# Kernel tuning notes

Hardware: AMD Instinct MI355X
Metric: run time of the kernel (lower is better)

Reference implementation:

```python
import jax, jax.numpy as jnp
import numpy as np

L, P, B, C, H, W = 2, 2, 4, 128, 64, 64
K = 2  # negatives per sample


def setup_inputs() -> dict:
    key = jax.random.key(0)
    k1, k2, k3, k4, k5 = jax.random.split(key, 5)
    shp = (L, P, B, C, H, W)
    return {
        "style_E": jax.random.normal(k1, shp, dtype=jnp.float32),
        "style_S": jax.random.normal(k2, shp, dtype=jnp.float32),
        "translate_E": jax.random.normal(k3, shp, dtype=jnp.float32),
        "translate_S": jax.random.normal(k4, shp, dtype=jnp.float32),
        "neg_idx": jax.random.randint(k5, (B, K), 0, B, dtype=jnp.int32),
    }


def reference(style_E, style_S, translate_E, translate_S, neg_idx):
    # Stack E and S levels: [2L, P, B, C, N] with N = H*W
    S = jnp.concatenate([style_E, style_S], axis=0).reshape(2 * L, P, B, C, -1)
    T = jnp.concatenate([translate_E, translate_S], axis=0).reshape(2 * L, P, B, C, -1)

    # EFDM: sort style values; permute them to trans's rank order, then MSE.
    Vs = jnp.sort(S, axis=-1)                      # value_style
    idx_t = jnp.argsort(T, axis=-1)                # index_trans
    inv = jnp.argsort(idx_t, axis=-1)              # inverse_index

    # Positive pairs: style[b] vs trans[b]
    matched_pos = jnp.take_along_axis(Vs, inv, axis=-1)
    # mse over (C, N) per slice (matches mse_loss on a [1,C,N] tensor)
    pos = jnp.mean((T - matched_pos) ** 2, axis=(3, 4))  # [2L, P, B]
    poss_loss = pos.sum(axis=(0, 1))                      # [B]

    # Negatives: style[nb] vs trans[b] for nb in neg_idx[b]
    Vs_neg = Vs[:, :, neg_idx]                            # [2L, P, B, K, C, N]
    matched_neg = jnp.take_along_axis(Vs_neg, inv[:, :, :, None], axis=-1)
    neg = jnp.mean((T[:, :, :, None] - matched_neg) ** 2, axis=(4, 5))  # [2L, P, B, K]
    neg_loss = neg.sum(axis=(0, 1, 3))                    # [B]

    return jnp.sum(poss_loss / neg_loss)
```

## Files before the change

kernel.cpp:

```cpp
#include <hip/hip_runtime.h>


typedef unsigned int u32;
typedef __fp16 f16x2 __attribute__((ext_vector_type(2)));

constexpr int N     = 4096;
constexpr int NTH   = 256;
constexpr int CDIM  = 128;
constexpr int BDIM  = 4;
constexpr int KNEG  = 2;
constexpr int ROWS  = 4096;
constexpr int HALF  = 2048;
constexpr int LSTRW = 20;
constexpr int ROWW  = N / 2;

__device__ inline u32 pk_min(u32 a, u32 b) {
  u32 d; asm("v_pk_min_f16 %0, %1, %2" : "=v"(d) : "v"(a), "v"(b)); return d;
}
__device__ inline u32 pk_max(u32 a, u32 b) {
  u32 d; asm("v_pk_max_f16 %0, %1, %2" : "=v"(d) : "v"(a), "v"(b)); return d;
}
__device__ inline u32 pk_min_swap(u32 a) {
  u32 d; asm("v_pk_min_f16 %0, %1, %1 op_sel:[0,1] op_sel_hi:[1,0]" : "=v"(d) : "v"(a)); return d;
}
__device__ inline u32 pk_max_swap(u32 a) {
  u32 d; asm("v_pk_max_f16 %0, %1, %1 op_sel:[0,1] op_sel_hi:[1,0]" : "=v"(d) : "v"(a)); return d;
}
__device__ inline u32 pk_sub(u32 a, u32 b) {
  u32 d; asm("v_pk_add_f16 %0, %1, %2 neg_lo:[0,1] neg_hi:[0,1]" : "=v"(d) : "v"(a), "v"(b)); return d;
}
__device__ inline float dot2acc(u32 d, float acc) {
  asm("v_dot2_f32_f16 %0, %1, %2, %0" : "+v"(acc) : "v"(d), "v"(d)); return acc;
}

__device__ inline void pk_cswap(u32& a, u32& b) {
  const u32 mn = pk_min(a, b), mx = pk_max(a, b);
  a = mn; b = mx;
}
__device__ inline u32 pk_sort_pair(u32 a) {
  const u32 mn = pk_min_swap(a);
  const u32 mx = pk_max_swap(a);
  return (mx & 0xFFFF0000u) | (mn & 0x0000FFFFu);
}

__device__ inline void cswap_asc(float& a, float& b) {
  const float lo = fminf(a, b), hi = fmaxf(a, b);
  a = lo; b = hi;
}
template<int K, int J>
__device__ inline void local_pass(float v[16]) {
  #pragma unroll
  for (int m = 0; m < 16; ++m)
    if ((m & J) == 0) {
      if ((m & K) == 0) cswap_asc(v[m], v[m ^ J]);
      else              cswap_asc(v[m ^ J], v[m]);
    }
}

template<int CTRL>
__device__ inline u32 dpp_u(u32 x) {
  return (u32)__builtin_amdgcn_update_dpp((int)x, (int)x, CTRL, 0xF, 0xF, false);
}

template<int TM>
__device__ inline void pass_small_pk(u32 h[8], int t) {
  const bool km = ((t & TM) == 0);
  u32 o[8];
  #pragma unroll
  for (int p = 0; p < 8; ++p) {
    if constexpr (TM == 1)      o[p] = dpp_u<0xB1>(h[p]);
    else if constexpr (TM == 2) o[p] = dpp_u<0x4E>(h[p]);
    else if constexpr (TM == 4) o[p] = dpp_u<0x141>(dpp_u<0x1B>(h[p]));
    else                        o[p] = dpp_u<0x128>(h[p]);
  }
  #pragma unroll
  for (int p = 0; p < 8; ++p) {
    const u32 mn = pk_min(h[p], o[p]), mx = pk_max(h[p], o[p]);
    h[p] = km ? mn : mx;
  }
}

__device__ inline void swap32u(u32& a, u32& b) {
  asm("v_permlane32_swap_b32 %0, %1" : "+v"(a), "+v"(b));
}
__device__ inline void swap16u(u32& a, u32& b) {
  asm("v_permlane16_swap_b32 %0, %1" : "+v"(a), "+v"(b));
}
template<bool IS32>
__device__ inline void pass_perm_pk(u32 h[8]) {
  #pragma unroll
  for (int q = 0; q < 4; ++q) {
    u32 a = h[2*q], b = h[2*q + 1];
    if constexpr (IS32) swap32u(a, b); else swap16u(a, b);
    u32 mn = pk_min(a, b);
    u32 mx = pk_max(a, b);
    if constexpr (IS32) swap32u(mn, mx); else swap16u(mn, mx);
    h[2*q] = mn; h[2*q + 1] = mx;
  }
}

template<int TM>
__device__ inline void pass_lds_pk(u32 h[8], u32* buf, int t) {
  __syncthreads();
  uint4* wp = (uint4*)(buf + t * LSTRW);
  wp[0] = make_uint4(h[0], h[1], h[2], h[3]);
  wp[1] = make_uint4(h[4], h[5], h[6], h[7]);
  __syncthreads();
  const uint4* rp = (const uint4*)(buf + (t ^ TM) * LSTRW);
  const uint4 x0 = rp[0], x1 = rp[1];
  if (t & TM) {
    h[0] = pk_max(h[0], x0.x); h[1] = pk_max(h[1], x0.y);
    h[2] = pk_max(h[2], x0.z); h[3] = pk_max(h[3], x0.w);
    h[4] = pk_max(h[4], x1.x); h[5] = pk_max(h[5], x1.y);
    h[6] = pk_max(h[6], x1.z); h[7] = pk_max(h[7], x1.w);
  } else {
    h[0] = pk_min(h[0], x0.x); h[1] = pk_min(h[1], x0.y);
    h[2] = pk_min(h[2], x0.z); h[3] = pk_min(h[3], x0.w);
    h[4] = pk_min(h[4], x1.x); h[5] = pk_min(h[5], x1.y);
    h[6] = pk_min(h[6], x1.z); h[7] = pk_min(h[7], x1.w);
  }
}

template<int K, int J>
__device__ inline void cross_pk(u32 h[8], u32* buf, int t) {
  if constexpr (J >= 16) {
    constexpr int TM = J >> 4;
    if constexpr (TM >= 64)      pass_lds_pk<TM>(h, buf, t);
    else if constexpr (TM == 32) pass_perm_pk<true>(h);
    else if constexpr (TM == 16) pass_perm_pk<false>(h);
    else                         pass_small_pk<TM>(h, t);
    cross_pk<K, (J >> 1)>(h, buf, t);
  }
}

__device__ inline void tail_pk(u32 h[8]) {
  #pragma unroll
  for (int p = 0; p < 8; ++p) h[p] = pk_sort_pair(h[p]);
  pk_cswap(h[0], h[4]); pk_cswap(h[1], h[5]); pk_cswap(h[2], h[6]); pk_cswap(h[3], h[7]);
  pk_cswap(h[0], h[2]); pk_cswap(h[1], h[3]); pk_cswap(h[4], h[6]); pk_cswap(h[5], h[7]);
  pk_cswap(h[0], h[1]); pk_cswap(h[2], h[3]); pk_cswap(h[4], h[5]); pk_cswap(h[6], h[7]);
}

__device__ inline void flip_pk(u32 h[8], u32 f) {
  #pragma unroll
  for (int p = 0; p < 8; ++p) h[p] ^= f;
}

template<int K>
__device__ inline void stage_pk(u32 h[8], u32* buf, int t, u32& cur) {
  const u32 f = (t & (K >> 4)) ? 0x80008000u : 0u;
  flip_pk(h, f ^ cur);
  cur = f;
  cross_pk<K, (K >> 1)>(h, buf, t);
  tail_pk(h);
}

__device__ inline void load_prestage_pack(const float* __restrict__ src,
                                          u32 h[8], int t) {
  float v[16];
  const float4* s4 = (const float4*)src;
  #pragma unroll
  for (int q = 0; q < 4; ++q) {
    const float4 x = s4[t * 4 + q];
    v[q*4+0] = x.x; v[q*4+1] = x.y; v[q*4+2] = x.z; v[q*4+3] = x.w;
  }
  local_pass<2, 1>(v);
  local_pass<4, 2>(v); local_pass<4, 1>(v);
  local_pass<8, 4>(v); local_pass<8, 2>(v); local_pass<8, 1>(v);
  #pragma unroll
  for (int p = 0; p < 8; ++p) {
    const f16x2 pk = __builtin_amdgcn_cvt_pkrtz(v[p], v[p + 8]);
    h[p] = __builtin_bit_cast(u32, pk);
  }
}

__device__ inline void sort4096_pk(u32 h[8], u32* buf, int t) {
  u32 cur = 0;
  stage_pk<16>(h, buf, t, cur);
  stage_pk<32>(h, buf, t, cur);
  stage_pk<64>(h, buf, t, cur);
  stage_pk<128>(h, buf, t, cur);
  stage_pk<256>(h, buf, t, cur);
  stage_pk<512>(h, buf, t, cur);
  stage_pk<1024>(h, buf, t, cur);
  stage_pk<2048>(h, buf, t, cur);
  stage_pk<4096>(h, buf, t, cur);
}

__device__ inline void store_row(u32* __restrict__ dst, const u32 h[8], int t) {
  uint4* d4 = (uint4*)dst;
  d4[t*2]     = make_uint4(h[0], h[1], h[2], h[3]);
  d4[t*2 + 1] = make_uint4(h[4], h[5], h[6], h[7]);
}

__global__ __launch_bounds__(NTH)
void sort_one(const float* __restrict__ sE, const float* __restrict__ sS,
              const float* __restrict__ tE, const float* __restrict__ tS,
              u32* __restrict__ Ss, u32* __restrict__ Ts) {
  __shared__ u32 buf[NTH * LSTRW];
  const int t = threadIdx.x;
  int r = blockIdx.x;
  const float* src;
  u32* dst;
  if (r < ROWS) {
    src = (r < HALF) ? sE + (size_t)r * N : sS + (size_t)(r - HALF) * N;
    dst = Ss + (size_t)r * ROWW;
  } else {
    r -= ROWS;
    src = (r < HALF) ? tE + (size_t)r * N : tS + (size_t)(r - HALF) * N;
    dst = Ts + (size_t)r * ROWW;
  }
  u32 h[8];
  load_prestage_pack(src, h, t);
  sort4096_pk(h, buf, t);
  store_row(dst, h, t);
}

__global__ __launch_bounds__(NTH)
void diff_rows(const u32* __restrict__ Ss, const u32* __restrict__ Ts,
               const int* __restrict__ neg_idx, float2* __restrict__ partial) {
  __shared__ float red[2][4];
  const int t = threadIdx.x, r = blockIdx.x;

  const uint4* tp = (const uint4*)(Ts + (size_t)r * ROWW);
  const uint4 h0 = tp[t*2], h1 = tp[t*2 + 1];

  const int c  = r & (CDIM - 1);
  const int b  = (r / CDIM) & (BDIM - 1);
  const int ap = r / (CDIM * BDIM);

  float posp = 0.f, negp = 0.f;
  {
    const uint4* vp = (const uint4*)(Ss + (size_t)r * ROWW);
    const uint4 w0 = vp[t*2], w1 = vp[t*2 + 1];
    posp = dot2acc(pk_sub(h0.x, w0.x), posp);
    posp = dot2acc(pk_sub(h0.y, w0.y), posp);
    posp = dot2acc(pk_sub(h0.z, w0.z), posp);
    posp = dot2acc(pk_sub(h0.w, w0.w), posp);
    posp = dot2acc(pk_sub(h1.x, w1.x), posp);
    posp = dot2acc(pk_sub(h1.y, w1.y), posp);
    posp = dot2acc(pk_sub(h1.z, w1.z), posp);
    posp = dot2acc(pk_sub(h1.w, w1.w), posp);
  }
  #pragma unroll
  for (int k = 0; k < KNEG; ++k) {
    const int nb = neg_idx[b * KNEG + k];
    const uint4* vp = (const uint4*)(Ss + ((size_t)(ap * BDIM + nb) * CDIM + c) * ROWW);
    const uint4 w0 = vp[t*2], w1 = vp[t*2 + 1];
    negp = dot2acc(pk_sub(h0.x, w0.x), negp);
    negp = dot2acc(pk_sub(h0.y, w0.y), negp);
    negp = dot2acc(pk_sub(h0.z, w0.z), negp);
    negp = dot2acc(pk_sub(h0.w, w0.w), negp);
    negp = dot2acc(pk_sub(h1.x, w1.x), negp);
    negp = dot2acc(pk_sub(h1.y, w1.y), negp);
    negp = dot2acc(pk_sub(h1.z, w1.z), negp);
    negp = dot2acc(pk_sub(h1.w, w1.w), negp);
  }

  #pragma unroll
  for (int off = 32; off > 0; off >>= 1) {
    posp += __shfl_down(posp, off, 64);
    negp += __shfl_down(negp, off, 64);
  }
  const int wid = t >> 6, lane = t & 63;
  if (lane == 0) { red[0][wid] = posp; red[1][wid] = negp; }
  __syncthreads();
  if (t == 0) {
    const float pt = red[0][0] + red[0][1] + red[0][2] + red[0][3];
    const float nt = red[1][0] + red[1][1] + red[1][2] + red[1][3];
    partial[r] = make_float2(pt, nt);
  }
}

__global__ __launch_bounds__(NTH)
void finalize(const float2* __restrict__ partial, float* __restrict__ out) {
  __shared__ double rp[4], rn[4];
  const int t = threadIdx.x;
  const int wid = t >> 6, lane = t & 63;
  double res = 0.0;
  #pragma unroll
  for (int b = 0; b < BDIM; ++b) {
    double p = 0.0, n = 0.0;
    for (int idx = t; idx < 1024; idx += NTH) {
      const int a = idx >> 7, c = idx & 127;
      const float2 v = partial[a * 512 + b * 128 + c];
      p += (double)v.x; n += (double)v.y;
    }
    #pragma unroll
    for (int off = 32; off > 0; off >>= 1) {
      p += __shfl_down(p, off, 64);
      n += __shfl_down(n, off, 64);
    }
    if (lane == 0) { rp[wid] = p; rn[wid] = n; }
    __syncthreads();
    if (t == 0) {
      const double P = rp[0] + rp[1] + rp[2] + rp[3];
      const double Nn = rn[0] + rn[1] + rn[2] + rn[3];
      res += P / Nn;
    }
    __syncthreads();
  }
  if (t == 0) out[0] = (float)res;
}

extern "C" void kernel_launch(void* const* d_in, const int* in_sizes, int n_in,
                              void* d_out, int out_size, void* d_ws, size_t ws_size,
                              hipStream_t stream) {
  const float* style_E = (const float*)d_in[0];
  const float* style_S = (const float*)d_in[1];
  const float* trans_E = (const float*)d_in[2];
  const float* trans_S = (const float*)d_in[3];
  const int*   neg_idx = (const int*)d_in[4];

  u32*    Ss      = (u32*)d_ws;
  u32*    Ts      = Ss + (size_t)ROWS * ROWW;
  float2* partial = (float2*)(Ts + (size_t)ROWS * ROWW);

  sort_one<<<2 * ROWS, NTH, 0, stream>>>(style_E, style_S, trans_E, trans_S, Ss, Ts);
  diff_rows<<<ROWS, NTH, 0, stream>>>(Ss, Ts, neg_idx, partial);
  finalize<<<1, NTH, 0, stream>>>(partial, (float*)d_out);
}
```

Measured before the change: 124.7 us.

## Use sign-flip polarity trick for DPP bitonic passes and packed prestage sort

New measurement: 119.0 us. 1.05x faster.

```diff
diff --git a/kernel.cpp b/kernel.cpp
--- a/kernel.cpp
+++ b/kernel.cpp
@@ -11,14 +11,19 @@
 constexpr int KNEG  = 2;
 constexpr int ROWS  = 4096;
 constexpr int HALF  = 2048;
-constexpr int LSTRW = 20;
 constexpr int ROWW  = N / 2;
+
+__device__ inline int lslot(int t) { return t * 16 + ((t >> 3) << 2); }
+constexpr int LDSW = 4224;
 
 __device__ inline u32 pk_min(u32 a, u32 b) {
   u32 d; asm("v_pk_min_f16 %0, %1, %2" : "=v"(d) : "v"(a), "v"(b)); return d;
 }
 __device__ inline u32 pk_max(u32 a, u32 b) {
   u32 d; asm("v_pk_max_f16 %0, %1, %2" : "=v"(d) : "v"(a), "v"(b)); return d;
+}
+__device__ inline u32 pk_min_negb(u32 a, u32 b) {
+  u32 d; asm("v_pk_min_f16 %0, %1, %2 neg_lo:[0,1] neg_hi:[0,1]" : "=v"(d) : "v"(a), "v"(b)); return d;
 }
 __device__ inline u32 pk_min_swap(u32 a) {
   u32 d; asm("v_pk_min_f16 %0, %1, %1 op_sel:[0,1] op_sel_hi:[1,0]" : "=v"(d) : "v"(a)); return d;
@@ -43,41 +48,16 @@
   return (mx & 0xFFFF0000u) | (mn & 0x0000FFFFu);
 }
 
-__device__ inline void cswap_asc(float& a, float& b) {
-  const float lo = fminf(a, b), hi = fmaxf(a, b);
-  a = lo; b = hi;
-}
-template<int K, int J>
-__device__ inline void local_pass(float v[16]) {
-  #pragma unroll
-  for (int m = 0; m < 16; ++m)
-    if ((m & J) == 0) {
-      if ((m & K) == 0) cswap_asc(v[m], v[m ^ J]);
-      else              cswap_asc(v[m ^ J], v[m]);
-    }
-}
-
 template<int CTRL>
 __device__ inline u32 dpp_u(u32 x) {
   return (u32)__builtin_amdgcn_update_dpp((int)x, (int)x, CTRL, 0xF, 0xF, false);
 }
-
 template<int TM>
-__device__ inline void pass_small_pk(u32 h[8], int t) {
-  const bool km = ((t & TM) == 0);
-  u32 o[8];
-  #pragma unroll
-  for (int p = 0; p < 8; ++p) {
-    if constexpr (TM == 1)      o[p] = dpp_u<0xB1>(h[p]);
-    else if constexpr (TM == 2) o[p] = dpp_u<0x4E>(h[p]);
-    else if constexpr (TM == 4) o[p] = dpp_u<0x141>(dpp_u<0x1B>(h[p]));
-    else                        o[p] = dpp_u<0x128>(h[p]);
-  }
-  #pragma unroll
-  for (int p = 0; p < 8; ++p) {
-    const u32 mn = pk_min(h[p], o[p]), mx = pk_max(h[p], o[p]);
-    h[p] = km ? mn : mx;
-  }
+__device__ inline u32 dppx(u32 x) {
+  if constexpr (TM == 1)      return dpp_u<0xB1>(x);
+  else if constexpr (TM == 2) return dpp_u<0x4E>(x);
+  else if constexpr (TM == 4) return dpp_u<0x141>(dpp_u<0x1B>(x));
+  else                        return dpp_u<0x128>(x);
 }
 
 __device__ inline void swap32u(u32& a, u32& b) {
@@ -99,14 +79,43 @@
   }
 }
 
+__device__ inline void flip_pk(u32 h[8], u32 f) {
+  #pragma unroll
+  for (int p = 0; p < 8; ++p) h[p] ^= f;
+}
+
+struct PolM { u32 s1, s2, s4, s8; };
+
+template<int TM>
+__device__ inline void polar_pass(u32 h[8]) {
+  u32 o[8];
+  #pragma unroll
+  for (int p = 0; p < 8; ++p) o[p] = dppx<TM>(h[p]);
+  #pragma unroll
+  for (int p = 0; p < 8; ++p) h[p] = pk_min_negb(h[p], o[p]);
+}
+
+template<int TMS, bool SKIP_ENTRY>
+__device__ inline void polar_block(u32 h[8], const PolM& pm) {
+  if constexpr (!SKIP_ENTRY) {
+    const u32 e = (TMS == 8) ? pm.s8 : (TMS == 4) ? pm.s4 : (TMS == 2) ? pm.s2 : pm.s1;
+    flip_pk(h, e);
+  }
+  if constexpr (TMS >= 8) { polar_pass<8>(h); flip_pk(h, pm.s8 ^ pm.s4); }
+  if constexpr (TMS >= 4) { polar_pass<4>(h); flip_pk(h, pm.s4 ^ pm.s2); }
+  if constexpr (TMS >= 2) { polar_pass<2>(h); flip_pk(h, pm.s2 ^ pm.s1); }
+  polar_pass<1>(h);
+  flip_pk(h, pm.s1);
+}
+
 template<int TM>
 __device__ inline void pass_lds_pk(u32 h[8], u32* buf, int t) {
   __syncthreads();
-  uint4* wp = (uint4*)(buf + t * LSTRW);
+  uint4* wp = (uint4*)(buf + lslot(t));
   wp[0] = make_uint4(h[0], h[1], h[2], h[3]);
   wp[1] = make_uint4(h[4], h[5], h[6], h[7]);
   __syncthreads();
-  const uint4* rp = (const uint4*)(buf + (t ^ TM) * LSTRW);
+  const uint4* rp = (const uint4*)(buf + lslot(t ^ TM));
   const uint4 x0 = rp[0], x1 = rp[1];
   if (t & TM) {
     h[0] = pk_max(h[0], x0.x); h[1] = pk_max(h[1], x0.y);
@@ -121,18 +130,6 @@
   }
 }
 
-template<int K, int J>
-__device__ inline void cross_pk(u32 h[8], u32* buf, int t) {
-  if constexpr (J >= 16) {
-    constexpr int TM = J >> 4;
-    if constexpr (TM >= 64)      pass_lds_pk<TM>(h, buf, t);
-    else if constexpr (TM == 32) pass_perm_pk<true>(h);
-    else if constexpr (TM == 16) pass_perm_pk<false>(h);
-    else                         pass_small_pk<TM>(h, t);
-    cross_pk<K, (J >> 1)>(h, buf, t);
-  }
-}
-
 __device__ inline void tail_pk(u32 h[8]) {
   #pragma unroll
   for (int p = 0; p < 8; ++p) h[p] = pk_sort_pair(h[p]);
@@ -141,17 +138,23 @@
   pk_cswap(h[0], h[1]); pk_cswap(h[2], h[3]); pk_cswap(h[4], h[5]); pk_cswap(h[6], h[7]);
 }
 
-__device__ inline void flip_pk(u32 h[8], u32 f) {
-  #pragma unroll
-  for (int p = 0; p < 8; ++p) h[p] ^= f;
-}
-
 template<int K>
-__device__ inline void stage_pk(u32 h[8], u32* buf, int t, u32& cur) {
-  const u32 f = (t & (K >> 4)) ? 0x80008000u : 0u;
-  flip_pk(h, f ^ cur);
+__device__ inline void stage_pk(u32 h[8], u32* buf, int t, u32& cur, const PolM& pm) {
+  constexpr bool FOLD = (K >= 32 && K <= 256);
+  const u32 f = (K >= 4096) ? 0u : ((t & (K >> 4)) ? 0x80008000u : 0u);
+  u32 m = f ^ cur;
+  if constexpr (FOLD)
+    m ^= (K == 256) ? pm.s8 : (K == 128) ? pm.s4 : (K == 64) ? pm.s2 : pm.s1;
+  flip_pk(h, m);
   cur = f;
-  cross_pk<K, (K >> 1)>(h, buf, t);
+  if constexpr (K >= 4096) pass_lds_pk<128>(h, buf, t);
+  if constexpr (K >= 2048) pass_lds_pk<64>(h, buf, t);
+  if constexpr (K >= 1024) pass_perm_pk<true>(h);
+  if constexpr (K >= 512)  pass_perm_pk<false>(h);
+  if constexpr (K >= 256)      polar_block<8, FOLD>(h, pm);
+  else if constexpr (K >= 128) polar_block<4, FOLD>(h, pm);
+  else if constexpr (K >= 64)  polar_block<2, FOLD>(h, pm);
+  else if constexpr (K >= 32)  polar_block<1, FOLD>(h, pm);
   tail_pk(h);
 }
 
@@ -161,43 +164,42 @@
   const float4* s4 = (const float4*)src;
   #pragma unroll
   for (int q = 0; q < 4; ++q) {
-    const float4 x = s4[t * 4 + q];
+    const float4 x = s4[t*4 + q];
     v[q*4+0] = x.x; v[q*4+1] = x.y; v[q*4+2] = x.z; v[q*4+3] = x.w;
   }
-  local_pass<2, 1>(v);
-  local_pass<4, 2>(v); local_pass<4, 1>(v);
-  local_pass<8, 4>(v); local_pass<8, 2>(v); local_pass<8, 1>(v);
   #pragma unroll
   for (int p = 0; p < 8; ++p) {
     const f16x2 pk = __builtin_amdgcn_cvt_pkrtz(v[p], v[p + 8]);
     h[p] = __builtin_bit_cast(u32, pk);
   }
-}
-
-__device__ inline void sort4096_pk(u32 h[8], u32* buf, int t) {
-  u32 cur = 0;
-  stage_pk<16>(h, buf, t, cur);
-  stage_pk<32>(h, buf, t, cur);
-  stage_pk<64>(h, buf, t, cur);
-  stage_pk<128>(h, buf, t, cur);
-  stage_pk<256>(h, buf, t, cur);
-  stage_pk<512>(h, buf, t, cur);
-  stage_pk<1024>(h, buf, t, cur);
-  stage_pk<2048>(h, buf, t, cur);
-  stage_pk<4096>(h, buf, t, cur);
-}
-
-__device__ inline void store_row(u32* __restrict__ dst, const u32 h[8], int t) {
-  uint4* d4 = (uint4*)dst;
-  d4[t*2]     = make_uint4(h[0], h[1], h[2], h[3]);
-  d4[t*2 + 1] = make_uint4(h[4], h[5], h[6], h[7]);
+  pk_cswap(h[0], h[1]); pk_cswap(h[3], h[2]); pk_cswap(h[4], h[5]); pk_cswap(h[7], h[6]);
+  pk_cswap(h[0], h[2]); pk_cswap(h[1], h[3]); pk_cswap(h[6], h[4]); pk_cswap(h[7], h[5]);
+  pk_cswap(h[0], h[1]); pk_cswap(h[2], h[3]); pk_cswap(h[5], h[4]); pk_cswap(h[7], h[6]);
+  #pragma unroll
+  for (int p = 0; p < 8; ++p) h[p] ^= 0x80000000u;
+  pk_cswap(h[0], h[4]); pk_cswap(h[1], h[5]); pk_cswap(h[2], h[6]); pk_cswap(h[3], h[7]);
+  pk_cswap(h[0], h[2]); pk_cswap(h[1], h[3]); pk_cswap(h[4], h[6]); pk_cswap(h[5], h[7]);
+  pk_cswap(h[0], h[1]); pk_cswap(h[2], h[3]); pk_cswap(h[4], h[5]); pk_cswap(h[6], h[7]);
+}
+
+__device__ inline void sort4096_pk(u32 h[8], u32* buf, int t, const PolM& pm) {
+  u32 cur = 0x80000000u;
+  stage_pk<16>(h, buf, t, cur, pm);
+  stage_pk<32>(h, buf, t, cur, pm);
+  stage_pk<64>(h, buf, t, cur, pm);
+  stage_pk<128>(h, buf, t, cur, pm);
+  stage_pk<256>(h, buf, t, cur, pm);
+  stage_pk<512>(h, buf, t, cur, pm);
+  stage_pk<1024>(h, buf, t, cur, pm);
+  stage_pk<2048>(h, buf, t, cur, pm);
+  stage_pk<4096>(h, buf, t, cur, pm);
 }
 
 __global__ __launch_bounds__(NTH)
 void sort_one(const float* __restrict__ sE, const float* __restrict__ sS,
               const float* __restrict__ tE, const float* __restrict__ tS,
               u32* __restrict__ Ss, u32* __restrict__ Ts) {
-  __shared__ u32 buf[NTH * LSTRW];
+  __shared__ u32 buf[LDSW];
   const int t = threadIdx.x;
   int r = blockIdx.x;
   const float* src;
@@ -210,10 +212,17 @@
     src = (r < HALF) ? tE + (size_t)r * N : tS + (size_t)(r - HALF) * N;
     dst = Ts + (size_t)r * ROWW;
   }
+  const u32 S = 0x80008000u;
+  PolM pm;
+  pm.s1 = (t & 1) ? S : 0u;  pm.s2 = (t & 2) ? S : 0u;
+  pm.s4 = (t & 4) ? S : 0u;  pm.s8 = (t & 8) ? S : 0u;
+
   u32 h[8];
   load_prestage_pack(src, h, t);
-  sort4096_pk(h, buf, t);
-  store_row(dst, h, t);
+  sort4096_pk(h, buf, t, pm);
+  uint4* d4 = (uint4*)dst;
+  d4[t]       = make_uint4(h[0], h[1], h[2], h[3]);
+  d4[NTH + t] = make_uint4(h[4], h[5], h[6], h[7]);
 }
 
 __global__ __launch_bounds__(NTH)
@@ -223,7 +232,7 @@
   const int t = threadIdx.x, r = blockIdx.x;
 
   const uint4* tp = (const uint4*)(Ts + (size_t)r * ROWW);
-  const uint4 h0 = tp[t*2], h1 = tp[t*2 + 1];
+  const uint4 h0 = tp[t], h1 = tp[NTH + t];
 
   const int c  = r & (CDIM - 1);
   const int b  = (r / CDIM) & (BDIM - 1);
@@ -232,7 +241,7 @@
   float posp = 0.f, negp = 0.f;
   {
     const uint4* vp = (const uint4*)(Ss + (size_t)r * ROWW);
-    const uint4 w0 = vp[t*2], w1 = vp[t*2 + 1];
+    const uint4 w0 = vp[t], w1 = vp[NTH + t];
     posp = dot2acc(pk_sub(h0.x, w0.x), posp);
     posp = dot2acc(pk_sub(h0.y, w0.y), posp);
     posp = dot2acc(pk_sub(h0.z, w0.z), posp);
@@ -246,7 +255,7 @@
   for (int k = 0; k < KNEG; ++k) {
     const int nb = neg_idx[b * KNEG + k];
     const uint4* vp = (const uint4*)(Ss + ((size_t)(ap * BDIM + nb) * CDIM + c) * ROWW);
-    const uint4 w0 = vp[t*2], w1 = vp[t*2 + 1];
+    const uint4 w0 = vp[t], w1 = vp[NTH + t];
     negp = dot2acc(pk_sub(h0.x, w0.x), negp);
     negp = dot2acc(pk_sub(h0.y, w0.y), negp);
     negp = dot2acc(pk_sub(h0.z, w0.z), negp);
```
